# Kernel optimization log

Measured on AMD Instinct MI355X. Metric: run time of the kernel, lower is better.

## Reference

```python
import jax, jax.numpy as jnp
import numpy as np

KS = [3, 3, 7, 7, 11, 11, 21, 21]  # TEXT_KERNEL_SIZES
KMAX = 21
H = 8
D_MODEL = 1024
D_H = D_MODEL // H
R = 4
B = 2
N = 4096


def _extract_windows_1d(xh, k):
    # xh: (B, n, d_h) -> windows: (B, n, k, d_h), zero-padded, stride 1
    pad = k // 2
    xp = jnp.pad(xh, ((0, 0), (pad, pad), (0, 0)))
    idx = jnp.arange(xh.shape[1])[:, None] + jnp.arange(k)[None, :]  # (n, k)
    return xp[:, idx]  # (B, n, k, d_h)


def setup_inputs() -> dict:
    key = jax.random.key(0)
    ks = jax.random.split(key, 10)
    s = 0.02
    return {
        "x": jax.random.normal(ks[0], (B, N, D_MODEL), dtype=jnp.float32),
        "W_in": jax.random.normal(ks[1], (D_MODEL, D_MODEL), dtype=jnp.float32) * s,
        "b_in": jnp.zeros((D_MODEL,), dtype=jnp.float32),
        "W_out": jax.random.normal(ks[2], (D_MODEL, D_MODEL), dtype=jnp.float32) * (0.02 / np.sqrt(2.0 * 8)),
        "b_out": jnp.zeros((D_MODEL,), dtype=jnp.float32),
        "Wc": jax.random.normal(ks[3], (H, D_H, R), dtype=jnp.float32) * s,  # per-token coeff proj
        "A": jax.random.normal(ks[4], (H, R, KMAX), dtype=jnp.float32) * s,  # rank -> kernel-pos factor (padded to KMAX)
        "V": jax.random.normal(ks[5], (H, R, D_H), dtype=jnp.float32) * s,   # rank -> channel factor
        "base": jax.random.normal(ks[6], (H, KMAX, D_H), dtype=jnp.float32) * s,  # static kernel (padded)
        "alphas": jnp.zeros((H,), dtype=jnp.float32),  # sigmoid gate params
    }


def reference(x, W_in, b_in, W_out, b_out, Wc, A, V, base, alphas):
    Bsz, n, d = x.shape
    x_proj = x @ W_in.T + b_in                        # (B, n, d_model)
    x_heads = x_proj.reshape(Bsz, n, H, D_H)          # (B, n, H, d_h)
    head_outs = []
    for h in range(H):
        k = KS[h]
        x_h = x_heads[:, :, h, :]                     # (B, n, d_h)
        # Factored per-token kernel generation
        c = x_h @ Wc[h]                               # (B, n, R)
        dyn = jnp.einsum('bnr,rk,rd->bnkd', c, A[h, :, :k], V[h])  # (B, n, k, d_h)
        alpha = jax.nn.sigmoid(alphas[h])
        K_hat = alpha * dyn + (1.0 - alpha) * base[h, :k][None, None]  # (B, n, k, d_h)
        windows = _extract_windows_1d(x_h, k)         # (B, n, k, d_h)
        o_h = jnp.einsum('bnkd,bnkd->bnd', K_hat, windows)
        head_outs.append(o_h)
    concat = jnp.concatenate(head_outs, axis=-1)      # (B, n, d_model)
    return concat @ W_out.T + b_out
```

## Files before the change

kernel.cpp:

```cpp
#include <hip/hip_runtime.h>
#include <stdint.h>

typedef __bf16 bf16;
typedef __bf16 bf16x8 __attribute__((ext_vector_type(8)));
typedef float f32x4 __attribute__((ext_vector_type(4)));
typedef float f32x16 __attribute__((ext_vector_type(16)));

#define AS1 __attribute__((address_space(1)))
#define AS3 __attribute__((address_space(3)))

__device__ __forceinline__ void gload_lds16(const void* g, void* l) {
    __builtin_amdgcn_global_load_lds((const AS1 uint32_t*)g, (AS3 uint32_t*)l, 16, 0, 0);
}

#define BM 128
#define BN 128
#define BK 64

template <typename OT>
__global__ __launch_bounds__(256, 2) void gemm_nt(
    const bf16* __restrict__ A, const bf16* __restrict__ B,
    const float* __restrict__ bias, OT* __restrict__ C,
    int M, int N, int K)
{
    __shared__ bf16 smA[BM * BK];
    __shared__ bf16 smB[BN * BK];

    const int tid  = threadIdx.x;
    const int wave = tid >> 6;
    const int lane = tid & 63;
    const int wm = (wave >> 1) * 64;
    const int wn = (wave & 1) * 64;
    const int rowA0 = blockIdx.x * BM;
    const int rowB0 = blockIdx.y * BN;

    f32x16 acc[2][2] = {};

    const int l31 = lane & 31;
    const int khi = lane >> 5;

    for (int k0 = 0; k0 < K; k0 += BK) {
        #pragma unroll
        for (int i = 0; i < 4; ++i) {
            int slot = i * 256 + tid;
            int row  = slot >> 3;
            int kg   = slot & 7;
            int kd   = kg ^ ((row >> 1) & 7);
            gload_lds16(A + (size_t)(rowA0 + row) * K + k0 + kd * 8, &smA[slot * 8]);
            gload_lds16(B + (size_t)(rowB0 + row) * K + k0 + kd * 8, &smB[slot * 8]);
        }
        __syncthreads();

        #pragma unroll
        for (int s = 0; s < 4; ++s) {
            bf16x8 af[2], bfr[2];
            #pragma unroll
            for (int mi = 0; mi < 2; ++mi) {
                int row  = wm + mi * 32 + l31;
                int slot = row * 8 + ((s * 2 + khi) ^ ((row >> 1) & 7));
                af[mi] = *(const bf16x8*)&smA[slot * 8];
            }
            #pragma unroll
            for (int ni = 0; ni < 2; ++ni) {
                int row  = wn + ni * 32 + l31;
                int slot = row * 8 + ((s * 2 + khi) ^ ((row >> 1) & 7));
                bfr[ni] = *(const bf16x8*)&smB[slot * 8];
            }
            #pragma unroll
            for (int mi = 0; mi < 2; ++mi)
                #pragma unroll
                for (int ni = 0; ni < 2; ++ni)
                    acc[mi][ni] = __builtin_amdgcn_mfma_f32_32x32x16_bf16(
                        af[mi], bfr[ni], acc[mi][ni], 0, 0, 0);
        }
        __syncthreads();
    }

    #pragma unroll
    for (int ni = 0; ni < 2; ++ni) {
        int col = rowB0 + wn + ni * 32 + l31;
        float bcol = bias[col];
        #pragma unroll
        for (int mi = 0; mi < 2; ++mi) {
            #pragma unroll
            for (int r = 0; r < 16; ++r) {
                int row32 = (r & 3) + 8 * (r >> 2) + 4 * khi;
                int rowc  = rowA0 + wm + mi * 32 + row32;
                C[(size_t)rowc * N + col] = (OT)(acc[mi][ni][r] + bcol);
            }
        }
    }
}

__global__ void cast_all_kernel(const float* __restrict__ x, bf16* __restrict__ xb,
                                const float* __restrict__ wi, bf16* __restrict__ wib,
                                const float* __restrict__ wo, bf16* __restrict__ wob)
{
    const int NX8 = (2 * 4096 * 1024) / 8;
    const int NW8 = (1024 * 1024) / 8;
    int i = blockIdx.x * 256 + threadIdx.x;
    const float* in; bf16* out; int idx;
    if (i < NX8)            { in = x;  out = xb;  idx = i; }
    else if (i < NX8 + NW8) { in = wi; out = wib; idx = i - NX8; }
    else                    { in = wo; out = wob; idx = i - NX8 - NW8; }
    const float4* p = (const float4*)in;
    float4 a = p[2 * idx], b = p[2 * idx + 1];
    bf16x8 o;
    o[0] = (bf16)a.x; o[1] = (bf16)a.y; o[2] = (bf16)a.z; o[3] = (bf16)a.w;
    o[4] = (bf16)b.x; o[5] = (bf16)b.y; o[6] = (bf16)b.z; o[7] = (bf16)b.w;
    *(bf16x8*)(out + 8 * idx) = o;
}

__global__ __launch_bounds__(256) void c_compute(
    const bf16* __restrict__ xpb, const float* __restrict__ Wc,
    float* __restrict__ cbuf)
{
    const int wave = threadIdx.x >> 6, lane = threadIdx.x & 63;
    const int row  = blockIdx.x * 4 + wave;
    const int h    = lane >> 3;
    const int d0   = (lane & 7) * 16;

    const bf16* xr = xpb + (size_t)row * 1024 + lane * 16;
    bf16x8 v0 = *(const bf16x8*)xr;
    bf16x8 v1 = *(const bf16x8*)(xr + 8);
    float p0 = 0.f, p1 = 0.f, p2 = 0.f, p3 = 0.f;
    #pragma unroll
    for (int i = 0; i < 16; ++i) {
        float xv = (i < 8) ? (float)v0[i & 7] : (float)v1[i & 7];
        float4 wr = *(const float4*)(Wc + h * 512 + (d0 + i) * 4);
        p0 += xv * wr.x; p1 += xv * wr.y; p2 += xv * wr.z; p3 += xv * wr.w;
    }
    #pragma unroll
    for (int off = 1; off <= 4; off <<= 1) {
        p0 += __shfl_xor(p0, off);
        p1 += __shfl_xor(p1, off);
        p2 += __shfl_xor(p2, off);
        p3 += __shfl_xor(p3, off);
    }
    if ((lane & 7) == 0) {
        float4 o = {p0, p1, p2, p3};
        *(float4*)(cbuf + (size_t)row * 32 + h * 4) = o;
    }
}

__constant__ int KS_c[8] = {3, 3, 7, 7, 11, 11, 21, 21};

template <int K>
__device__ __forceinline__ void mix_body5(
    int h, int tid, int r0, const bf16* __restrict__ xpb,
    const float* __restrict__ cbuf, const float* __restrict__ Aw,
    const float* __restrict__ Vw, const float* __restrict__ basew,
    float alpha, bf16* __restrict__ y, bf16* sx, float* sB)
{
    constexpr int T   = 8;
    constexpr int pad = K / 2;
    constexpr int R   = 16 + 2 * pad;
    constexpr int SX  = R * 16;
    constexpr int SB  = K * 32;

    #pragma unroll
    for (int p = 0; p < (SX + 255) / 256; ++p) {
        int slot = p * 256 + tid;
        if (slot < SX) {
            int lrow = slot >> 4;
            int grow = min(max(r0 - pad + lrow, 0), 8191);
            gload_lds16(xpb + (size_t)grow * 1024 + h * 128 + (slot & 15) * 8,
                        sx + slot * 8);
        }
    }
    #pragma unroll
    for (int p = 0; p < (SB + 255) / 256; ++p) {
        int slot = p * 256 + tid;
        if (slot < SB)
            gload_lds16(basew + h * 2688 + slot * 4, sB + slot * 4);
    }
    __syncthreads();

    const int d   = tid & 127;
    const int sub = tid >> 7;
    const int lr0 = sub * 8;
    const int nb  = (r0 & 4095) + sub * 8;

    float w[T + K - 1];
    #pragma unroll
    for (int j = 0; j < T + K - 1; ++j) {
        int nl = nb + j - pad;
        float v = (float)sx[(lr0 + j) * 128 + d];
        w[j] = (nl >= 0 && nl < 4096) ? v : 0.f;
    }

    float s0[T] = {}, s1[T] = {}, s2[T] = {}, s3[T] = {}, tv[T] = {};
    const float* Ah = Aw + h * 84;
    #pragma unroll
    for (int j = 0; j < K; ++j) {
        float a0 = Ah[j], a1 = Ah[21 + j], a2 = Ah[42 + j], a3 = Ah[63 + j];
        float bbj = sB[j * 128 + d];
        #pragma unroll
        for (int t = 0; t < T; ++t) {
            float x = w[t + j];
            s0[t] += a0 * x; s1[t] += a1 * x;
            s2[t] += a2 * x; s3[t] += a3 * x;
            tv[t] += bbj * x;
        }
    }

    float v0 = Vw[h * 512 + d],       v1 = Vw[h * 512 + 128 + d];
    float v2 = Vw[h * 512 + 256 + d], v3 = Vw[h * 512 + 384 + d];
    #pragma unroll
    for (int t = 0; t < T; ++t) {
        int rowo = r0 + sub * 8 + t;
        float4 c4 = *(const float4*)(cbuf + (size_t)rowo * 32 + h * 4);
        float o = alpha * (c4.x * v0 * s0[t] + c4.y * v1 * s1[t] +
                           c4.z * v2 * s2[t] + c4.w * v3 * s3[t])
                + (1.f - alpha) * tv[t];
        y[(size_t)rowo * 1024 + h * 128 + d] = (bf16)o;
    }
}

__global__ __launch_bounds__(256, 4) void head_mix5(
    const bf16* __restrict__ xpb, const float* __restrict__ cbuf,
    const float* __restrict__ Aw, const float* __restrict__ Vw,
    const float* __restrict__ basew, const float* __restrict__ alphas,
    bf16* __restrict__ y)
{
    __shared__ __align__(16) bf16  sx[36 * 128];
    __shared__ __align__(16) float sB[21 * 128];
    const int h  = blockIdx.y;
    const int r0 = blockIdx.x * 16;
    const float alpha = 1.f / (1.f + __expf(-alphas[h]));

    switch (KS_c[h]) {
        case 3:  mix_body5<3 >(h, threadIdx.x, r0, xpb, cbuf, Aw, Vw, basew, alpha, y, sx, sB); break;
        case 7:  mix_body5<7 >(h, threadIdx.x, r0, xpb, cbuf, Aw, Vw, basew, alpha, y, sx, sB); break;
        case 11: mix_body5<11>(h, threadIdx.x, r0, xpb, cbuf, Aw, Vw, basew, alpha, y, sx, sB); break;
        default: mix_body5<21>(h, threadIdx.x, r0, xpb, cbuf, Aw, Vw, basew, alpha, y, sx, sB); break;
    }
}

extern "C" void kernel_launch(void* const* d_in, const int* in_sizes, int n_in,
                              void* d_out, int out_size, void* d_ws, size_t ws_size,
                              hipStream_t stream)
{
    const float* x      = (const float*)d_in[0];
    const float* W_in   = (const float*)d_in[1];
    const float* b_in   = (const float*)d_in[2];
    const float* W_out  = (const float*)d_in[3];
    const float* b_out  = (const float*)d_in[4];
    const float* Wc     = (const float*)d_in[5];
    const float* Aw     = (const float*)d_in[6];
    const float* Vw     = (const float*)d_in[7];
    const float* basew  = (const float*)d_in[8];
    const float* alphas = (const float*)d_in[9];
    float* out = (float*)d_out;

    const size_t MB = 1u << 20;
    char* ws = (char*)d_ws;
    bf16*  xb   = (bf16*) (ws);
    bf16*  wib  = (bf16*) (ws + 16 * MB);
    bf16*  wob  = (bf16*) (ws + 18 * MB);
    bf16*  xpb  = (bf16*) (ws + 20 * MB);
    bf16*  yb   = (bf16*) (ws + 36 * MB);
    float* cbuf = (float*)(ws + 52 * MB);

    const int NTOT8 = (2 * 4096 * 1024 + 2 * 1024 * 1024) / 8;

    cast_all_kernel<<<NTOT8 / 256, 256, 0, stream>>>(x, xb, W_in, wib, W_out, wob);

    gemm_nt<bf16><<<dim3(8192 / BM, 1024 / BN), 256, 0, stream>>>(
        xb, wib, b_in, xpb, 8192, 1024, 1024);

    c_compute<<<8192 / 4, 256, 0, stream>>>(xpb, Wc, cbuf);

    head_mix5<<<dim3(512, 8), 256, 0, stream>>>(
        xpb, cbuf, Aw, Vw, basew, alphas, yb);

    gemm_nt<float><<<dim3(8192 / BM, 1024 / BN), 256, 0, stream>>>(
        yb, wob, b_out, out, 8192, 1024, 1024);
}
```

Baseline: 179.8 us.

## Fuse coefficient projection into head-mix kernel and double GEMM K-tile

Removes the separate c_compute launch and its cbuf round-trip through global memory. The per-token coefficients are now computed inside the head-mix kernel from the x tile already staged in LDS, using a wave-wide shuffle reduction, and kept in shared memory. Separately, the GEMM K-tile grows from 64 to 128 with a 16-way XOR swizzle, halving the barrier count per K loop. The larger tile doubles LDS per block (64 KB), which may lower GEMM occupancy below the requested two blocks per CU.

```diff
diff --git a/kernel.cpp b/kernel.cpp
--- a/kernel.cpp
+++ b/kernel.cpp
@@ -15,7 +15,7 @@
 
 #define BM 128
 #define BN 128
-#define BK 64
+#define BK 128
 
 template <typename OT>
 __global__ __launch_bounds__(256, 2) void gemm_nt(
@@ -41,29 +41,29 @@
 
     for (int k0 = 0; k0 < K; k0 += BK) {
         #pragma unroll
-        for (int i = 0; i < 4; ++i) {
+        for (int i = 0; i < 8; ++i) {
             int slot = i * 256 + tid;
-            int row  = slot >> 3;
-            int kg   = slot & 7;
-            int kd   = kg ^ ((row >> 1) & 7);
+            int row  = slot >> 4;
+            int kg   = slot & 15;
+            int kd   = kg ^ ((row >> 1) & 15);
             gload_lds16(A + (size_t)(rowA0 + row) * K + k0 + kd * 8, &smA[slot * 8]);
             gload_lds16(B + (size_t)(rowB0 + row) * K + k0 + kd * 8, &smB[slot * 8]);
         }
         __syncthreads();
 
         #pragma unroll
-        for (int s = 0; s < 4; ++s) {
+        for (int s = 0; s < 8; ++s) {
             bf16x8 af[2], bfr[2];
             #pragma unroll
             for (int mi = 0; mi < 2; ++mi) {
                 int row  = wm + mi * 32 + l31;
-                int slot = row * 8 + ((s * 2 + khi) ^ ((row >> 1) & 7));
+                int slot = row * 16 + ((s * 2 + khi) ^ ((row >> 1) & 15));
                 af[mi] = *(const bf16x8*)&smA[slot * 8];
             }
             #pragma unroll
             for (int ni = 0; ni < 2; ++ni) {
                 int row  = wn + ni * 32 + l31;
-                int slot = row * 8 + ((s * 2 + khi) ^ ((row >> 1) & 7));
+                int slot = row * 16 + ((s * 2 + khi) ^ ((row >> 1) & 15));
                 bfr[ni] = *(const bf16x8*)&smB[slot * 8];
             }
             #pragma unroll
@@ -111,46 +111,14 @@
     *(bf16x8*)(out + 8 * idx) = o;
 }
 
-__global__ __launch_bounds__(256) void c_compute(
-    const bf16* __restrict__ xpb, const float* __restrict__ Wc,
-    float* __restrict__ cbuf)
-{
-    const int wave = threadIdx.x >> 6, lane = threadIdx.x & 63;
-    const int row  = blockIdx.x * 4 + wave;
-    const int h    = lane >> 3;
-    const int d0   = (lane & 7) * 16;
-
-    const bf16* xr = xpb + (size_t)row * 1024 + lane * 16;
-    bf16x8 v0 = *(const bf16x8*)xr;
-    bf16x8 v1 = *(const bf16x8*)(xr + 8);
-    float p0 = 0.f, p1 = 0.f, p2 = 0.f, p3 = 0.f;
-    #pragma unroll
-    for (int i = 0; i < 16; ++i) {
-        float xv = (i < 8) ? (float)v0[i & 7] : (float)v1[i & 7];
-        float4 wr = *(const float4*)(Wc + h * 512 + (d0 + i) * 4);
-        p0 += xv * wr.x; p1 += xv * wr.y; p2 += xv * wr.z; p3 += xv * wr.w;
-    }
-    #pragma unroll
-    for (int off = 1; off <= 4; off <<= 1) {
-        p0 += __shfl_xor(p0, off);
-        p1 += __shfl_xor(p1, off);
-        p2 += __shfl_xor(p2, off);
-        p3 += __shfl_xor(p3, off);
-    }
-    if ((lane & 7) == 0) {
-        float4 o = {p0, p1, p2, p3};
-        *(float4*)(cbuf + (size_t)row * 32 + h * 4) = o;
-    }
-}
-
 __constant__ int KS_c[8] = {3, 3, 7, 7, 11, 11, 21, 21};
 
 template <int K>
-__device__ __forceinline__ void mix_body5(
+__device__ __forceinline__ void mix_body6(
     int h, int tid, int r0, const bf16* __restrict__ xpb,
-    const float* __restrict__ cbuf, const float* __restrict__ Aw,
+    const float* __restrict__ Wc, const float* __restrict__ Aw,
     const float* __restrict__ Vw, const float* __restrict__ basew,
-    float alpha, bf16* __restrict__ y, bf16* sx, float* sB)
+    float alpha, bf16* __restrict__ y, bf16* sx, float* sB, float* sc)
 {
     constexpr int T   = 8;
     constexpr int pad = K / 2;
@@ -176,6 +144,36 @@
     }
     __syncthreads();
 
+    {
+        const int wv = tid >> 6, lane = tid & 63;
+        float4 w0 = *(const float4*)(Wc + h * 512 + lane * 4);
+        float4 w1 = *(const float4*)(Wc + h * 512 + (64 + lane) * 4);
+        #pragma unroll
+        for (int q = 0; q < 4; ++q) {
+            int lrow = pad + wv * 4 + q;
+            float x0 = (float)sx[lrow * 128 + lane];
+            float x1 = (float)sx[lrow * 128 + 64 + lane];
+            float p0 = x0 * w0.x + x1 * w1.x;
+            float p1 = x0 * w0.y + x1 * w1.y;
+            float p2 = x0 * w0.z + x1 * w1.z;
+            float p3 = x0 * w0.w + x1 * w1.w;
+            #pragma unroll
+            for (int off = 1; off < 64; off <<= 1) {
+                p0 += __shfl_xor(p0, off);
+                p1 += __shfl_xor(p1, off);
+                p2 += __shfl_xor(p2, off);
+                p3 += __shfl_xor(p3, off);
+            }
+            if (lane == 0) {
+                sc[(wv * 4 + q) * 4 + 0] = p0;
+                sc[(wv * 4 + q) * 4 + 1] = p1;
+                sc[(wv * 4 + q) * 4 + 2] = p2;
+                sc[(wv * 4 + q) * 4 + 3] = p3;
+            }
+        }
+    }
+    __syncthreads();
+
     const int d   = tid & 127;
     const int sub = tid >> 7;
     const int lr0 = sub * 8;
@@ -209,31 +207,35 @@
     #pragma unroll
     for (int t = 0; t < T; ++t) {
         int rowo = r0 + sub * 8 + t;
-        float4 c4 = *(const float4*)(cbuf + (size_t)rowo * 32 + h * 4);
-        float o = alpha * (c4.x * v0 * s0[t] + c4.y * v1 * s1[t] +
-                           c4.z * v2 * s2[t] + c4.w * v3 * s3[t])
+        float c0 = sc[(sub * 8 + t) * 4 + 0];
+        float c1 = sc[(sub * 8 + t) * 4 + 1];
+        float c2 = sc[(sub * 8 + t) * 4 + 2];
+        float c3 = sc[(sub * 8 + t) * 4 + 3];
+        float o = alpha * (c0 * v0 * s0[t] + c1 * v1 * s1[t] +
+                           c2 * v2 * s2[t] + c3 * v3 * s3[t])
                 + (1.f - alpha) * tv[t];
         y[(size_t)rowo * 1024 + h * 128 + d] = (bf16)o;
     }
 }
 
-__global__ __launch_bounds__(256, 4) void head_mix5(
-    const bf16* __restrict__ xpb, const float* __restrict__ cbuf,
+__global__ __launch_bounds__(256, 4) void head_mix6(
+    const bf16* __restrict__ xpb, const float* __restrict__ Wc,
     const float* __restrict__ Aw, const float* __restrict__ Vw,
     const float* __restrict__ basew, const float* __restrict__ alphas,
     bf16* __restrict__ y)
 {
     __shared__ __align__(16) bf16  sx[36 * 128];
     __shared__ __align__(16) float sB[21 * 128];
+    __shared__ float sc[16 * 4];
     const int h  = blockIdx.y;
     const int r0 = blockIdx.x * 16;
     const float alpha = 1.f / (1.f + __expf(-alphas[h]));
 
     switch (KS_c[h]) {
-        case 3:  mix_body5<3 >(h, threadIdx.x, r0, xpb, cbuf, Aw, Vw, basew, alpha, y, sx, sB); break;
-        case 7:  mix_body5<7 >(h, threadIdx.x, r0, xpb, cbuf, Aw, Vw, basew, alpha, y, sx, sB); break;
-        case 11: mix_body5<11>(h, threadIdx.x, r0, xpb, cbuf, Aw, Vw, basew, alpha, y, sx, sB); break;
-        default: mix_body5<21>(h, threadIdx.x, r0, xpb, cbuf, Aw, Vw, basew, alpha, y, sx, sB); break;
+        case 3:  mix_body6<3 >(h, threadIdx.x, r0, xpb, Wc, Aw, Vw, basew, alpha, y, sx, sB, sc); break;
+        case 7:  mix_body6<7 >(h, threadIdx.x, r0, xpb, Wc, Aw, Vw, basew, alpha, y, sx, sB, sc); break;
+        case 11: mix_body6<11>(h, threadIdx.x, r0, xpb, Wc, Aw, Vw, basew, alpha, y, sx, sB, sc); break;
+        default: mix_body6<21>(h, threadIdx.x, r0, xpb, Wc, Aw, Vw, basew, alpha, y, sx, sB, sc); break;
     }
 }
 
@@ -260,7 +262,6 @@
     bf16*  wob  = (bf16*) (ws + 18 * MB);
     bf16*  xpb  = (bf16*) (ws + 20 * MB);
     bf16*  yb   = (bf16*) (ws + 36 * MB);
-    float* cbuf = (float*)(ws + 52 * MB);
 
     const int NTOT8 = (2 * 4096 * 1024 + 2 * 1024 * 1024) / 8;
 
@@ -269,10 +270,8 @@
     gemm_nt<bf16><<<dim3(8192 / BM, 1024 / BN), 256, 0, stream>>>(
         xb, wib, b_in, xpb, 8192, 1024, 1024);
 
-    c_compute<<<8192 / 4, 256, 0, stream>>>(xpb, Wc, cbuf);
-
-    head_mix5<<<dim3(512, 8), 256, 0, stream>>>(
-        xpb, cbuf, Aw, Vw, basew, alphas, yb);
+    head_mix6<<<dim3(512, 8), 256, 0, stream>>>(
+        xpb, Wc, Aw, Vw, basew, alphas, yb);
 
     gemm_nt<float><<<dim3(8192 / BM, 1024 / BN), 256, 0, stream>>>(
         yb, wob, b_out, out, 8192, 1024, 1024);
```

Measured after the change: 172.5 us. -4.1%, faster.
